# Optimization experiments

Hardware: AMD Instinct MI355X
Metric: run time of the kernel (lower is better)

The kernel has to match this reference:

```python
import jax, jax.numpy as jnp
import numpy as np

DT = 0.01
NOISE_STD = 0.1
B, N = 65536, 1024


def setup_inputs() -> dict:
    key = jax.random.key(0)
    k1, k2, k3, k4 = jax.random.split(key, 4)
    theta = jax.random.normal(k1, (B, N), dtype=jnp.float32)
    noise = jax.random.normal(k2, (B, N), dtype=jnp.float32)
    omega = jax.random.normal(k3, (N,), dtype=jnp.float32) * 0.1
    K = jax.random.normal(k4, (N, N), dtype=jnp.float32) * 0.01
    return {"theta": theta, "noise": noise, "omega": omega, "K": K}


def reference(theta, noise, omega, K):
    # couplings[b,i] = sum_j K[i,j] * sin(theta[b,j] - theta[b,i])
    #               = cos(theta_i) * (sin(theta) @ K^T)_i - sin(theta_i) * (cos(theta) @ K^T)_i
    s = jnp.sin(theta)  # (B, N)
    c = jnp.cos(theta)  # (B, N)
    Ks = jnp.einsum("bj,ij->bi", s, K)  # (B, N)
    Kc = jnp.einsum("bj,ij->bi", c, K)  # (B, N)
    couplings = c * Ks - s * Kc
    dtheta = (omega + couplings) * DT
    noise_scale = NOISE_STD * float(np.sqrt(DT))
    return theta + dtheta + noise * noise_scale
```

## Files before the change

### kernel.cpp

```cpp
#include <hip/hip_runtime.h>
#include <hip/hip_bf16.h>
#include <math.h>

#define B_DIM 65536
#define N_DIM 1024
#define BM 64
#define BN 256
#define BK 64
#define NKT (N_DIM / BK)
#define THREADS 512
#define DT_C 0.01f
#define NS_SCALE 0.01f
#define KSCALE (127.0f / 0.08f)
#define DEQ (0.08f / (127.0f * 127.0f))
#define INV2PI 0.15915494309189535f

typedef __attribute__((ext_vector_type(4))) int   i32x4;
typedef __attribute__((ext_vector_type(4))) float f32x4;

__device__ __forceinline__ void gload_lds16(const void* g, void* l) {
    __builtin_amdgcn_global_load_lds(
        (const __attribute__((address_space(1))) void*)g,
        (__attribute__((address_space(3))) void*)l, 16, 0, 0);
}

__global__ __launch_bounds__(256)
void k_tileK(const float* __restrict__ K, signed char* __restrict__ KqT) {
    const int j  = blockIdx.x * 256 + threadIdx.x;
    const int c  = j >> 6;
    const int gr = j & 63;
    const float* src = K + (size_t)c * N_DIM + gr * 16;
    float4 v0 = *reinterpret_cast<const float4*>(src);
    float4 v1 = *reinterpret_cast<const float4*>(src + 4);
    float4 v2 = *reinterpret_cast<const float4*>(src + 8);
    float4 v3 = *reinterpret_cast<const float4*>(src + 12);
    float in[16] = {v0.x, v0.y, v0.z, v0.w, v1.x, v1.y, v1.z, v1.w,
                    v2.x, v2.y, v2.z, v2.w, v3.x, v3.y, v3.z, v3.w};
    int q[16];
#pragma unroll
    for (int e = 0; e < 16; ++e)
        q[e] = __float2int_rn(fminf(fmaxf(in[e] * KSCALE, -127.f), 127.f));
    int4 p;
    p.x = (q[0]  & 255) | ((q[1]  & 255) << 8) | ((q[2]  & 255) << 16) | (q[3]  << 24);
    p.y = (q[4]  & 255) | ((q[5]  & 255) << 8) | ((q[6]  & 255) << 16) | (q[7]  << 24);
    p.z = (q[8]  & 255) | ((q[9]  & 255) << 8) | ((q[10] & 255) << 16) | (q[11] << 24);
    p.w = (q[12] & 255) | ((q[13] & 255) << 8) | ((q[14] & 255) << 16) | (q[15] << 24);
    *reinterpret_cast<int4*>(KqT + ((size_t)gr * 1024 + c) * 16) = p;
}

__global__ __launch_bounds__(THREADS, 2)
void k_fused(const float* __restrict__ theta,
             const float* __restrict__ noise,
             const float* __restrict__ omega,
             const signed char* __restrict__ KqT,
             float* __restrict__ out) {
    __shared__ signed char sA[2][2][4][BM][16];
    __shared__ signed char sB[2][4][BN][16];

    const int tid  = threadIdx.x;
    const int lane = tid & 63;
    const int w    = tid >> 6;
    const int wm   = w >> 2;
    const int wn   = w & 3;
    const int lr   = lane & 15;
    const int kq   = lane >> 4;

    const int nwg     = gridDim.x;
    const int cpx     = nwg >> 3;
    const int logical = (blockIdx.x & 7) * cpx + (blockIdx.x >> 3);
    const int mt      = logical >> 2;
    const int nt      = logical & 3;
    const int row0    = mt * BM;
    const int col0    = nt * BN;

    const int ar = w * 8 + (lane >> 3);
    const int ag = (lane & 7) >> 1;
    const int ah = lane & 1;

    i32x4 accS[2][4], accC[2][4];
#pragma unroll
    for (int ms = 0; ms < 2; ++ms)
#pragma unroll
        for (int nf = 0; nf < 4; ++nf) {
            accS[ms][nf] = (i32x4){0, 0, 0, 0};
            accC[ms][nf] = (i32x4){0, 0, 0, 0};
        }

    auto stage = [&](int buf, int kt) {
#pragma unroll
        for (int i = 0; i < 2; ++i) {
            const int g  = i * 2 + (tid >> 8);
            const int rb = (w & 3) * 64;
            const signed char* src =
                KqT + ((size_t)(kt * 4 + g) * 1024 + col0 + rb + lane) * 16;
            gload_lds16(src, &sB[buf][g][rb][0]);
        }
        const float* gp = theta + (size_t)(row0 + ar) * N_DIM + kt * BK + (lane & 7) * 8;
        float4 v0 = *reinterpret_cast<const float4*>(gp);
        float4 v1 = *reinterpret_cast<const float4*>(gp + 4);
        float in[8] = {v0.x, v0.y, v0.z, v0.w, v1.x, v1.y, v1.z, v1.w};
        int qs[8], qc[8];
#pragma unroll
        for (int e = 0; e < 8; ++e) {
            const float rev = in[e] * INV2PI;
            qs[e] = __float2int_rn(__builtin_amdgcn_sinf(rev) * 127.f);
            qc[e] = __float2int_rn(__builtin_amdgcn_cosf(rev) * 127.f);
        }
        uint2 ps, pc;
        ps.x = (qs[0] & 255) | ((qs[1] & 255) << 8) | ((qs[2] & 255) << 16) | (qs[3] << 24);
        ps.y = (qs[4] & 255) | ((qs[5] & 255) << 8) | ((qs[6] & 255) << 16) | (qs[7] << 24);
        pc.x = (qc[0] & 255) | ((qc[1] & 255) << 8) | ((qc[2] & 255) << 16) | (qc[3] << 24);
        pc.y = (qc[4] & 255) | ((qc[5] & 255) << 8) | ((qc[6] & 255) << 16) | (qc[7] << 24);
        *reinterpret_cast<uint2*>(&sA[buf][0][ag][ar][ah * 8]) = ps;
        *reinterpret_cast<uint2*>(&sA[buf][1][ag][ar][ah * 8]) = pc;
    };

    auto compute = [&](int buf) {
        i32x4 aS[2], aC[2], bF[4];
#pragma unroll
        for (int ms = 0; ms < 2; ++ms) {
            aS[ms] = *reinterpret_cast<const i32x4*>(&sA[buf][0][kq][wm * 32 + ms * 16 + lr][0]);
            aC[ms] = *reinterpret_cast<const i32x4*>(&sA[buf][1][kq][wm * 32 + ms * 16 + lr][0]);
        }
#pragma unroll
        for (int nf = 0; nf < 4; ++nf)
            bF[nf] = *reinterpret_cast<const i32x4*>(&sB[buf][kq][wn * 64 + nf * 16 + lr][0]);
#pragma unroll
        for (int nf = 0; nf < 4; ++nf)
#pragma unroll
            for (int ms = 0; ms < 2; ++ms) {
                accS[ms][nf] = __builtin_amdgcn_mfma_i32_16x16x64_i8(aS[ms], bF[nf], accS[ms][nf], 0, 0, 0);
                accC[ms][nf] = __builtin_amdgcn_mfma_i32_16x16x64_i8(aC[ms], bF[nf], accC[ms][nf], 0, 0, 0);
            }
    };

    stage(0, 0);
    __syncthreads();
    int cur = 0;
    for (int kt = 0; kt < NKT; ++kt) {
        if (kt + 1 < NKT) stage(cur ^ 1, kt + 1);
        compute(cur);
        __syncthreads();
        cur ^= 1;
    }

    const int colbase = col0 + wn * 64 + lr;
    float om[4];
#pragma unroll
    for (int nf = 0; nf < 4; ++nf) om[nf] = omega[colbase + nf * 16];

#pragma unroll
    for (int ms = 0; ms < 2; ++ms) {
        const int rowg0 = row0 + wm * 32 + ms * 16 + kq * 4;
        float th[16], nz[16];
#pragma unroll
        for (int v = 0; v < 4; ++v) {
#pragma unroll
            for (int nf = 0; nf < 4; ++nf) {
                const size_t idx = (size_t)(rowg0 + v) * N_DIM + colbase + nf * 16;
                th[v * 4 + nf] = theta[idx];
                nz[v * 4 + nf] = noise[idx];
            }
        }
#pragma unroll
        for (int v = 0; v < 4; ++v) {
#pragma unroll
            for (int nf = 0; nf < 4; ++nf) {
                const size_t idx = (size_t)(rowg0 + v) * N_DIM + colbase + nf * 16;
                const float t  = th[v * 4 + nf];
                const float rev = t * INV2PI;
                const float sn = __builtin_amdgcn_sinf(rev);
                const float cn = __builtin_amdgcn_cosf(rev);
                const float coup =
                    (cn * (float)accS[ms][nf][v] - sn * (float)accC[ms][nf][v]) * DEQ;
                out[idx] = t + (om[nf] + coup) * DT_C + nz[v * 4 + nf] * NS_SCALE;
            }
        }
    }
}

extern "C" void kernel_launch(void* const* d_in, const int* in_sizes, int n_in,
                              void* d_out, int out_size, void* d_ws, size_t ws_size,
                              hipStream_t stream) {
    const float* theta = (const float*)d_in[0];
    const float* noise = (const float*)d_in[1];
    const float* omega = (const float*)d_in[2];
    const float* K     = (const float*)d_in[3];
    float* out = (float*)d_out;

    signed char* KqT = (signed char*)d_ws;
    k_tileK<<<(N_DIM * N_DIM / 16) / 256, 256, 0, stream>>>(K, KqT);

    const int grid = (B_DIM / BM) * (N_DIM / BN);
    k_fused<<<grid, THREADS, 0, stream>>>(theta, noise, omega, KqT, out);
}
```

Before: 302.6 us.

## Widen N tile to 512, swizzle A tile LDS rows, restructure epilogue loads

Doubles the output tile width per workgroup so each block covers half of N. The sin/cos quantization of theta is then recomputed two times per row instead of four, and each A fragment feeds twice as many MFMAs. It adds an XOR swizzle on the A tile rows in LDS to cut bank conflicts, and loads the epilogue operands one row at a time to keep register pressure down. The risk is 64 int32 accumulator registers per wave, which may reduce occupancy or cause spills under the two-blocks-per-CU launch bound.

```diff
diff --git a/kernel.cpp b/kernel.cpp
--- a/kernel.cpp
+++ b/kernel.cpp
@@ -5,7 +5,7 @@
 #define B_DIM 65536
 #define N_DIM 1024
 #define BM 64
-#define BN 256
+#define BN 512
 #define BK 64
 #define NKT (N_DIM / BK)
 #define THREADS 512
@@ -68,29 +68,31 @@
     const int nwg     = gridDim.x;
     const int cpx     = nwg >> 3;
     const int logical = (blockIdx.x & 7) * cpx + (blockIdx.x >> 3);
-    const int mt      = logical >> 2;
-    const int nt      = logical & 3;
+    const int mt      = logical >> 1;
+    const int nt      = logical & 1;
     const int row0    = mt * BM;
     const int col0    = nt * BN;
 
     const int ar = w * 8 + (lane >> 3);
     const int ag = (lane & 7) >> 1;
     const int ah = lane & 1;
+    const int arw = ar ^ (ag << 1);
 
-    i32x4 accS[2][4], accC[2][4];
+    i32x4 accS[2][8], accC[2][8];
 #pragma unroll
     for (int ms = 0; ms < 2; ++ms)
 #pragma unroll
-        for (int nf = 0; nf < 4; ++nf) {
+        for (int nf = 0; nf < 8; ++nf) {
             accS[ms][nf] = (i32x4){0, 0, 0, 0};
             accC[ms][nf] = (i32x4){0, 0, 0, 0};
         }
 
     auto stage = [&](int buf, int kt) {
 #pragma unroll
-        for (int i = 0; i < 2; ++i) {
-            const int g  = i * 2 + (tid >> 8);
-            const int rb = (w & 3) * 64;
+        for (int j = 0; j < 4; ++j) {
+            const int u  = w * 4 + j;
+            const int g  = u >> 3;
+            const int rb = (u & 7) * 64;
             const signed char* src =
                 KqT + ((size_t)(kt * 4 + g) * 1024 + col0 + rb + lane) * 16;
             gload_lds16(src, &sB[buf][g][rb][0]);
@@ -111,22 +113,23 @@
         ps.y = (qs[4] & 255) | ((qs[5] & 255) << 8) | ((qs[6] & 255) << 16) | (qs[7] << 24);
         pc.x = (qc[0] & 255) | ((qc[1] & 255) << 8) | ((qc[2] & 255) << 16) | (qc[3] << 24);
         pc.y = (qc[4] & 255) | ((qc[5] & 255) << 8) | ((qc[6] & 255) << 16) | (qc[7] << 24);
-        *reinterpret_cast<uint2*>(&sA[buf][0][ag][ar][ah * 8]) = ps;
-        *reinterpret_cast<uint2*>(&sA[buf][1][ag][ar][ah * 8]) = pc;
+        *reinterpret_cast<uint2*>(&sA[buf][0][ag][arw][ah * 8]) = ps;
+        *reinterpret_cast<uint2*>(&sA[buf][1][ag][arw][ah * 8]) = pc;
     };
 
     auto compute = [&](int buf) {
-        i32x4 aS[2], aC[2], bF[4];
+        i32x4 aS[2], aC[2], bF[8];
 #pragma unroll
         for (int ms = 0; ms < 2; ++ms) {
-            aS[ms] = *reinterpret_cast<const i32x4*>(&sA[buf][0][kq][wm * 32 + ms * 16 + lr][0]);
-            aC[ms] = *reinterpret_cast<const i32x4*>(&sA[buf][1][kq][wm * 32 + ms * 16 + lr][0]);
+            const int rrow = (wm * 32 + ms * 16 + lr) ^ (kq << 1);
+            aS[ms] = *reinterpret_cast<const i32x4*>(&sA[buf][0][kq][rrow][0]);
+            aC[ms] = *reinterpret_cast<const i32x4*>(&sA[buf][1][kq][rrow][0]);
         }
 #pragma unroll
-        for (int nf = 0; nf < 4; ++nf)
-            bF[nf] = *reinterpret_cast<const i32x4*>(&sB[buf][kq][wn * 64 + nf * 16 + lr][0]);
+        for (int nf = 0; nf < 8; ++nf)
+            bF[nf] = *reinterpret_cast<const i32x4*>(&sB[buf][kq][wn * 128 + nf * 16 + lr][0]);
 #pragma unroll
-        for (int nf = 0; nf < 4; ++nf)
+        for (int nf = 0; nf < 8; ++nf)
 #pragma unroll
             for (int ms = 0; ms < 2; ++ms) {
                 accS[ms][nf] = __builtin_amdgcn_mfma_i32_16x16x64_i8(aS[ms], bF[nf], accS[ms][nf], 0, 0, 0);
@@ -144,36 +147,34 @@
         cur ^= 1;
     }
 
-    const int colbase = col0 + wn * 64 + lr;
-    float om[4];
+    const int colbase = col0 + wn * 128 + lr;
+    float om[8];
 #pragma unroll
-    for (int nf = 0; nf < 4; ++nf) om[nf] = omega[colbase + nf * 16];
+    for (int nf = 0; nf < 8; ++nf) om[nf] = omega[colbase + nf * 16];
 
 #pragma unroll
     for (int ms = 0; ms < 2; ++ms) {
         const int rowg0 = row0 + wm * 32 + ms * 16 + kq * 4;
-        float th[16], nz[16];
 #pragma unroll
         for (int v = 0; v < 4; ++v) {
+            const size_t rowoff = (size_t)(rowg0 + v) * N_DIM;
+            float th[8], nz[8];
 #pragma unroll
-            for (int nf = 0; nf < 4; ++nf) {
-                const size_t idx = (size_t)(rowg0 + v) * N_DIM + colbase + nf * 16;
-                th[v * 4 + nf] = theta[idx];
-                nz[v * 4 + nf] = noise[idx];
+            for (int nf = 0; nf < 8; ++nf) {
+                const size_t idx = rowoff + colbase + nf * 16;
+                th[nf] = theta[idx];
+                nz[nf] = noise[idx];
             }
-        }
 #pragma unroll
-        for (int v = 0; v < 4; ++v) {
-#pragma unroll
-            for (int nf = 0; nf < 4; ++nf) {
-                const size_t idx = (size_t)(rowg0 + v) * N_DIM + colbase + nf * 16;
-                const float t  = th[v * 4 + nf];
+            for (int nf = 0; nf < 8; ++nf) {
+                const size_t idx = rowoff + colbase + nf * 16;
+                const float t  = th[nf];
                 const float rev = t * INV2PI;
                 const float sn = __builtin_amdgcn_sinf(rev);
                 const float cn = __builtin_amdgcn_cosf(rev);
                 const float coup =
                     (cn * (float)accS[ms][nf][v] - sn * (float)accC[ms][nf][v]) * DEQ;
-                out[idx] = t + (om[nf] + coup) * DT_C + nz[v * 4 + nf] * NS_SCALE;
+                out[idx] = t + (om[nf] + coup) * DT_C + nz[nf] * NS_SCALE;
             }
         }
     }
```

Result: slower. 375.3 us (+24.0%).
